# Optimization experiments

Measured on AMD Instinct MI355X. Metric: run time of the kernel, lower is better.

The kernel has to match this reference:

```python
import jax, jax.numpy as jnp
import numpy as np


def setup_inputs() -> dict:
    key = jax.random.key(0)
    ks = jax.random.split(key, 4)
    B, S, D, H, E = 4, 2048, 1024, 4096, 4
    sd = 1.0 / np.sqrt(D)
    sh = 1.0 / np.sqrt(H)
    return {
        "x": jax.random.normal(ks[0], (B, S, D), jnp.float32),
        "Wr": jax.random.normal(ks[1], (D, E), jnp.float32) * sd,
        "W1": jax.random.normal(ks[2], (E, D, H), jnp.float32) * sd,
        "b1": jnp.zeros((E, H), jnp.float32),
        "W2": jax.random.normal(ks[3], (E, H, D), jnp.float32) * sh,
        "b2": jnp.zeros((E, D), jnp.float32),
        "top_k": 2,
    }


def reference(x, Wr, W1, b1, W2, b2, top_k):
    # Router: softmax over experts, then top-k + renormalize (as in torch code)
    logits = jnp.einsum("bsd,de->bse", x, Wr)              # [B,S,E]
    probs = jax.nn.softmax(logits, axis=-1)
    wk, idx = jax.lax.top_k(probs, top_k)                  # [B,S,K]
    wk = wk / jnp.sum(wk, axis=-1, keepdims=True)
    # Scatter top-k weights back to dense per-expert weights [B,S,E]
    E = probs.shape[-1]
    onehot = jax.nn.one_hot(idx, E, dtype=x.dtype)         # [B,S,K,E]
    weights = jnp.einsum("bsk,bske->bse", wk, onehot)      # [B,S,E]
    # Expert MLPs (Linear-ReLU-Linear), computed dense over experts and
    # combined with the (mostly-zero) routing weights — same math as the
    # gather/scatter loop in the torch module.
    h = jax.nn.relu(jnp.einsum("bsd,edh->bseh", x, W1) + b1)   # [B,S,E,H]
    y = jnp.einsum("bseh,ehd->bsed", h, W2) + b2               # [B,S,E,D]
    out = jnp.einsum("bse,bsed->bsd", weights, y)              # [B,S,D]
    aux_loss = jnp.asarray(0.0, dtype=x.dtype)
    return out, aux_loss
```

## Files before the change

kernel.cpp:

```cpp
#include <hip/hip_runtime.h>
#include <cstdint>
#include <cstddef>

typedef _Float16 f16;
typedef __attribute__((ext_vector_type(8))) f16 f16x8;
typedef __attribute__((ext_vector_type(4))) f16 f16x4;
typedef __attribute__((ext_vector_type(4))) float f32x4;

#define M_TOK 8192
#define DDIM 1024
#define HDIM 4096
#define NEXP 4
#define TOTPAD 16896

__device__ __forceinline__ void async_copy16(const void* g, void* s) {
    __builtin_amdgcn_global_load_lds((__attribute__((address_space(1))) void*)g,
                                     (__attribute__((address_space(3))) void*)s,
                                     16, 0, 0);
}

__global__ __launch_bounds__(256) void router_kernel(
    const float* __restrict__ x, const float* __restrict__ Wr,
    float* __restrict__ wts, int* __restrict__ top2, float2* __restrict__ wpair) {
    __shared__ float wr_s[DDIM * NEXP];
    for (int i = threadIdx.x; i < DDIM * NEXP; i += 256) wr_s[i] = Wr[i];
    __syncthreads();
    const int wave = threadIdx.x >> 6, lane = threadIdx.x & 63;
    const int t = blockIdx.x * 4 + wave;
    float a0 = 0.f, a1 = 0.f, a2 = 0.f, a3 = 0.f;
    const float* xr = x + (size_t)t * DDIM;
    for (int i = 0; i < DDIM; i += 256) {
        const int d = i + lane * 4;
        const float4 v = *(const float4*)(xr + d);
        const float* w0 = &wr_s[d * 4];
        a0 += v.x * w0[0] + v.y * w0[4] + v.z * w0[8]  + v.w * w0[12];
        a1 += v.x * w0[1] + v.y * w0[5] + v.z * w0[9]  + v.w * w0[13];
        a2 += v.x * w0[2] + v.y * w0[6] + v.z * w0[10] + v.w * w0[14];
        a3 += v.x * w0[3] + v.y * w0[7] + v.z * w0[11] + v.w * w0[15];
    }
    for (int off = 32; off > 0; off >>= 1) {
        a0 += __shfl_xor(a0, off, 64);
        a1 += __shfl_xor(a1, off, 64);
        a2 += __shfl_xor(a2, off, 64);
        a3 += __shfl_xor(a3, off, 64);
    }
    if (lane == 0) {
        float lg[4] = {a0, a1, a2, a3};
        int i1 = 0;
        for (int e = 1; e < 4; ++e) if (lg[e] > lg[i1]) i1 = e;
        int i2 = -1;
        for (int e = 0; e < 4; ++e) {
            if (e == i1) continue;
            if (i2 < 0 || lg[e] > lg[i2]) i2 = e;
        }
        const float w1 = 1.0f / (1.0f + expf(lg[i2] - lg[i1]));
        float w[4] = {0.f, 0.f, 0.f, 0.f};
        w[i1] = w1; w[i2] = 1.0f - w1;
        float* o = wts + (size_t)t * 4;
        o[0] = w[0]; o[1] = w[1]; o[2] = w[2]; o[3] = w[3];
        top2[t] = i1 | (i2 << 8);
        wpair[t] = make_float2(w1, 1.0f - w1);
    }
}

__global__ __launch_bounds__(256) void count_kernel(
    const int* __restrict__ top2, int* __restrict__ meta) {
    __shared__ int lc[4];
    if (threadIdx.x < 4) lc[threadIdx.x] = 0;
    __syncthreads();
    const int t = blockIdx.x * 256 + threadIdx.x;
    const int p = top2[t];
    atomicAdd(&lc[p & 0xff], 1);
    atomicAdd(&lc[(p >> 8) & 0xff], 1);
    __syncthreads();
    if (threadIdx.x < 4) atomicAdd(&meta[threadIdx.x], lc[threadIdx.x]);
}

__global__ void offsets_kernel(int* __restrict__ meta) {
    if (threadIdx.x == 0) {
        int off = 0;
        for (int e = 0; e < 4; ++e) {
            const int c = meta[e];
            const int cp = (c + 127) & ~127;
            meta[4 + e] = cp;
            meta[8 + e] = off;
            off += cp;
        }
    }
}

__global__ __launch_bounds__(256) void fill_kernel(
    const int* __restrict__ top2, int* __restrict__ meta,
    int* __restrict__ toklist, int2* __restrict__ slotmap) {
    __shared__ int lc[4], base[4];
    if (threadIdx.x < 4) lc[threadIdx.x] = 0;
    __syncthreads();
    const int t = blockIdx.x * 256 + threadIdx.x;
    const int p = top2[t];
    const int e1 = p & 0xff, e2 = (p >> 8) & 0xff;
    const int r1 = atomicAdd(&lc[e1], 1);
    const int r2 = atomicAdd(&lc[e2], 1);
    __syncthreads();
    if (threadIdx.x < 4) base[threadIdx.x] = atomicAdd(&meta[12 + threadIdx.x], lc[threadIdx.x]);
    __syncthreads();
    const int p1 = meta[8 + e1] + base[e1] + r1;
    const int p2 = meta[8 + e2] + base[e2] + r2;
    toklist[p1] = t;
    toklist[p2] = t;
    slotmap[t] = make_int2(p1, p2);
}

__global__ __launch_bounds__(256) void convert_f16_kernel(
    const float* __restrict__ in, f16* __restrict__ out, int n4) {
    const int i = blockIdx.x * 256 + threadIdx.x;
    if (i < n4) {
        const float4 v = ((const float4*)in)[i];
        f16x4 o = {(f16)v.x, (f16)v.y, (f16)v.z, (f16)v.w};
        ((f16x4*)out)[i] = o;
    }
}

__global__ __launch_bounds__(256) void transpose_f16_kernel(
    const float* __restrict__ in0, f16* __restrict__ out0, int R, int C) {
    __shared__ float tile[32][33];
    const float* in = in0 + (size_t)blockIdx.z * R * C;
    f16* out = out0 + (size_t)blockIdx.z * R * C;
    const int c0 = blockIdx.x * 32, r0 = blockIdx.y * 32;
    const int tx = threadIdx.x & 31;
    const int ty = threadIdx.x >> 5;
#pragma unroll
    for (int i = 0; i < 32; i += 8)
        tile[ty + i][tx] = in[(size_t)(r0 + ty + i) * C + c0 + tx];
    __syncthreads();
#pragma unroll
    for (int i = 0; i < 32; i += 8)
        out[(size_t)(c0 + ty + i) * R + r0 + tx] = (f16)tile[tx][ty + i];
}

template <int MODE>
__global__ __launch_bounds__(256) void gemm_kernel(
    const f16* __restrict__ A, const f16* __restrict__ BT,
    int N, int K,
    const float* __restrict__ bias,
    f16* __restrict__ outH, float* __restrict__ outF,
    const float* __restrict__ wts,
    const int* __restrict__ toklist, const int* __restrict__ meta, int e0) {
    __shared__ __align__(16) f16 As[128 * 64];
    __shared__ __align__(16) f16 Bs[128 * 64];
    const int zz = blockIdx.z;
    const int e = e0 + zz;
    const int m0 = blockIdx.x * 128, n0 = blockIdx.y * 128;

    int cnt = M_TOK, off = 0;
    if (meta) {
        cnt = meta[e];
        const int cp = meta[4 + e];
        off = meta[8 + e];
        if (m0 >= cp) return;
    }

    const f16* BTe = BT + (size_t)zz * N * K;
    const float* be = bias + (size_t)zz * N;

    const int tid = threadIdx.x;
    const int wave = tid >> 6, lane = tid & 63;
    const int wm = wave >> 1, wn = wave & 1;
    const int quad = lane >> 4, l16 = lane & 15;

    f32x4 acc[4][4] = {};

    const int lrb = tid >> 3;
    const int gcoff = (((tid & 7) ^ (lrb & 7)) * 8);
    const f16* ga[4];
    const f16* gb[4];
#pragma unroll
    for (int r = 0; r < 4; ++r) {
        const int lr = r * 32 + lrb;
        const int gm = m0 + lr;
        int arow;
        if (MODE == 0) arow = toklist ? toklist[off + gm] : gm;
        else arow = off + gm;
        ga[r] = A + (size_t)arow * K + gcoff;
        gb[r] = BTe + (size_t)(n0 + lr) * K + gcoff;
    }

    const int swl = l16 & 7;
    for (int k0 = 0; k0 < K; k0 += 64) {
#pragma unroll
        for (int r = 0; r < 4; ++r)
            async_copy16(ga[r] + k0, &As[(r * 256 + tid) * 8]);
#pragma unroll
        for (int r = 0; r < 4; ++r)
            async_copy16(gb[r] + k0, &Bs[(r * 256 + tid) * 8]);
        __syncthreads();
#pragma unroll
        for (int kk = 0; kk < 64; kk += 32) {
            const int kc = kk >> 3;
            f16x8 af[4], bf[4];
#pragma unroll
            for (int i = 0; i < 4; ++i)
                af[i] = *(const f16x8*)&As[(size_t)(wm * 64 + i * 16 + l16) * 64 +
                                           (((kc + quad) ^ swl) << 3)];
#pragma unroll
            for (int j = 0; j < 4; ++j)
                bf[j] = *(const f16x8*)&Bs[(size_t)(wn * 64 + j * 16 + l16) * 64 +
                                           (((kc + quad) ^ swl) << 3)];
#pragma unroll
            for (int i = 0; i < 4; ++i)
#pragma unroll
                for (int j = 0; j < 4; ++j)
                    acc[i][j] = __builtin_amdgcn_mfma_f32_16x16x32_f16(af[i], bf[j], acc[i][j], 0, 0, 0);
        }
        __syncthreads();
    }

#pragma unroll
    for (int i = 0; i < 4; ++i) {
        const int mbase = m0 + wm * 64 + i * 16 + quad * 4;
#pragma unroll
        for (int j = 0; j < 4; ++j) {
            const int n = n0 + wn * 64 + j * 16 + l16;
            const float bv = be[n];
#pragma unroll
            for (int r = 0; r < 4; ++r) {
                const int m = mbase + r;
                float v = acc[i][j][r] + bv;
                if (MODE == 0) {
                    v = v > 0.0f ? v : 0.0f;
                    outH[(size_t)(off + m) * N + n] = (f16)v;
                } else {
                    if (outH) {
                        outH[(size_t)(off + m) * N + n] = (f16)v;
                    } else if (m < cnt) {
                        const float w = wts[m * 4 + e];
                        atomicAdd(&outF[(size_t)m * N + n], w * v);
                    }
                }
            }
        }
    }
}

__global__ __launch_bounds__(256) void combine_kernel(
    const f16* __restrict__ yseg, const int2* __restrict__ slotmap,
    const float2* __restrict__ wpair, float* __restrict__ out, int aux_idx) {
    const int t = blockIdx.x;
    const int2 p = slotmap[t];
    const float2 w = wpair[t];
    const int d = threadIdx.x * 4;
    const f16x4 a = *(const f16x4*)&yseg[(size_t)p.x * DDIM + d];
    const f16x4 b = *(const f16x4*)&yseg[(size_t)p.y * DDIM + d];
    float4 o;
    o.x = w.x * (float)a[0] + w.y * (float)b[0];
    o.y = w.x * (float)a[1] + w.y * (float)b[1];
    o.z = w.x * (float)a[2] + w.y * (float)b[2];
    o.w = w.x * (float)a[3] + w.y * (float)b[3];
    *(float4*)&out[(size_t)t * DDIM + d] = o;
    if (t == 0 && threadIdx.x == 0 && aux_idx >= 0) out[aux_idx] = 0.0f;
}

extern "C" void kernel_launch(void* const* d_in, const int* in_sizes, int n_in,
                              void* d_out, int out_size, void* d_ws, size_t ws_size,
                              hipStream_t stream) {
    (void)in_sizes; (void)n_in;
    const float* x  = (const float*)d_in[0];
    const float* Wr = (const float*)d_in[1];
    const float* W1 = (const float*)d_in[2];
    const float* b1 = (const float*)d_in[3];
    const float* W2 = (const float*)d_in[4];
    const float* b2 = (const float*)d_in[5];
    float* out = (float*)d_out;

    char* ws = (char*)d_ws;
    float*  wts   = (float*)ws;
    int*    meta  = (int*)(ws + (128 << 10));
    int*    top2  = (int*)(ws + (132 << 10));
    int*    tokl  = (int*)(ws + (164 << 10));
    float2* wpair = (float2*)(ws + (240 << 10));
    int2*   slotm = (int2*)(ws + (304 << 10));
    f16*    xb    = (f16*)(ws + (512 << 10));
    const size_t MBs = 1ull << 20;
    const size_t base = (512 << 10) + 16 * MBs;

    const size_t SPARSE_NEED = (512 << 10) + 80 * MBs + (size_t)TOTPAD * HDIM * sizeof(f16);
    const bool sparse = ws_size >= SPARSE_NEED;

    const int aux_idx = (out_size == M_TOK * DDIM + 1) ? (M_TOK * DDIM) : -1;

    f16 *w1t, *w2t, *h, *yseg;
    if (sparse) {
        w1t  = (f16*)(ws + base);
        w2t  = (f16*)(ws + base + 32 * MBs);
        h    = (f16*)(ws + base + 64 * MBs);
        yseg = (f16*)(ws + (512 << 10));
    } else {
        w1t = (f16*)(ws + base);
        w2t = (f16*)(ws + base + 8 * MBs);
        h   = (f16*)(ws + base + 16 * MBs);
        yseg = nullptr;
    }

    router_kernel<<<M_TOK / 4, 256, 0, stream>>>(x, Wr, wts, top2, wpair);
    convert_f16_kernel<<<(M_TOK * DDIM / 4) / 256, 256, 0, stream>>>(x, xb, M_TOK * DDIM / 4);

    if (sparse) {
        hipMemsetAsync(meta, 0, 16 * sizeof(int), stream);
        hipMemsetAsync(tokl, 0, (size_t)TOTPAD * sizeof(int), stream);
        count_kernel<<<M_TOK / 256, 256, 0, stream>>>(top2, meta);
        offsets_kernel<<<1, 64, 0, stream>>>(meta);
        fill_kernel<<<M_TOK / 256, 256, 0, stream>>>(top2, meta, tokl, slotm);
        transpose_f16_kernel<<<dim3(HDIM / 32, DDIM / 32, NEXP), 256, 0, stream>>>(W1, w1t, DDIM, HDIM);
        transpose_f16_kernel<<<dim3(DDIM / 32, HDIM / 32, NEXP), 256, 0, stream>>>(W2, w2t, HDIM, DDIM);
        gemm_kernel<0><<<dim3(M_TOK / 128, HDIM / 128, NEXP), 256, 0, stream>>>(
            xb, w1t, HDIM, DDIM, b1, h, nullptr, wts, tokl, meta, 0);
        gemm_kernel<1><<<dim3(M_TOK / 128, DDIM / 128, NEXP), 256, 0, stream>>>(
            h, w2t, DDIM, HDIM, b2, yseg, nullptr, wts, tokl, meta, 0);
        combine_kernel<<<M_TOK, 256, 0, stream>>>(yseg, slotm, wpair, out, aux_idx);
    } else {
        hipMemsetAsync(out, 0, (size_t)out_size * sizeof(float), stream);
        if (aux_idx < 0) {  }
        for (int e = 0; e < NEXP; ++e) {
            transpose_f16_kernel<<<dim3(HDIM / 32, DDIM / 32, 1), 256, 0, stream>>>(
                W1 + (size_t)e * DDIM * HDIM, w1t, DDIM, HDIM);
            gemm_kernel<0><<<dim3(M_TOK / 128, HDIM / 128, 1), 256, 0, stream>>>(
                xb, w1t, HDIM, DDIM, b1 + (size_t)e * HDIM, h, nullptr, wts, nullptr, nullptr, e);
            transpose_f16_kernel<<<dim3(DDIM / 32, HDIM / 32, 1), 256, 0, stream>>>(
                W2 + (size_t)e * HDIM * DDIM, w2t, HDIM, DDIM);
            gemm_kernel<1><<<dim3(M_TOK / 128, DDIM / 128, 1), 256, 0, stream>>>(
                h, w2t, DDIM, HDIM, b2 + (size_t)e * DDIM, nullptr, out, wts, nullptr, nullptr, e);
        }
    }
}
```

Measured before the change: 751.5 us.

## Double-buffer GEMM LDS tiles with register-staged prefetch of next K tile

```diff
diff --git a/kernel.cpp b/kernel.cpp
--- a/kernel.cpp
+++ b/kernel.cpp
@@ -6,18 +6,13 @@
 typedef __attribute__((ext_vector_type(8))) f16 f16x8;
 typedef __attribute__((ext_vector_type(4))) f16 f16x4;
 typedef __attribute__((ext_vector_type(4))) float f32x4;
+typedef __attribute__((ext_vector_type(4))) unsigned int u32x4;
 
 #define M_TOK 8192
 #define DDIM 1024
 #define HDIM 4096
 #define NEXP 4
 #define TOTPAD 16896
-
-__device__ __forceinline__ void async_copy16(const void* g, void* s) {
-    __builtin_amdgcn_global_load_lds((__attribute__((address_space(1))) void*)g,
-                                     (__attribute__((address_space(3))) void*)s,
-                                     16, 0, 0);
-}
 
 __global__ __launch_bounds__(256) void router_kernel(
     const float* __restrict__ x, const float* __restrict__ Wr,
@@ -138,15 +133,15 @@
 }
 
 template <int MODE>
-__global__ __launch_bounds__(256) void gemm_kernel(
+__global__ __launch_bounds__(256, 2) void gemm_kernel(
     const f16* __restrict__ A, const f16* __restrict__ BT,
     int N, int K,
     const float* __restrict__ bias,
     f16* __restrict__ outH, float* __restrict__ outF,
     const float* __restrict__ wts,
     const int* __restrict__ toklist, const int* __restrict__ meta, int e0) {
-    __shared__ __align__(16) f16 As[128 * 64];
-    __shared__ __align__(16) f16 Bs[128 * 64];
+    __shared__ __align__(16) f16 As[2][128 * 64];
+    __shared__ __align__(16) f16 Bs[2][128 * 64];
     const int zz = blockIdx.z;
     const int e = e0 + zz;
     const int m0 = blockIdx.x * 128, n0 = blockIdx.y * 128;
@@ -184,33 +179,49 @@
         gb[r] = BTe + (size_t)(n0 + lr) * K + gcoff;
     }
 
+    u32x4 ra[4], rb[4];
+#pragma unroll
+    for (int r = 0; r < 4; ++r) ra[r] = *(const u32x4*)(ga[r]);
+#pragma unroll
+    for (int r = 0; r < 4; ++r) rb[r] = *(const u32x4*)(gb[r]);
+#pragma unroll
+    for (int r = 0; r < 4; ++r) *(u32x4*)&As[0][(r * 256 + tid) * 8] = ra[r];
+#pragma unroll
+    for (int r = 0; r < 4; ++r) *(u32x4*)&Bs[0][(r * 256 + tid) * 8] = rb[r];
+    __syncthreads();
+
     const int swl = l16 & 7;
     for (int k0 = 0; k0 < K; k0 += 64) {
-#pragma unroll
-        for (int r = 0; r < 4; ++r)
-            async_copy16(ga[r] + k0, &As[(r * 256 + tid) * 8]);
-#pragma unroll
-        for (int r = 0; r < 4; ++r)
-            async_copy16(gb[r] + k0, &Bs[(r * 256 + tid) * 8]);
-        __syncthreads();
+        const int p = (k0 >> 6) & 1;
+        const int kn = (k0 + 64 < K) ? (k0 + 64) : 0;
+#pragma unroll
+        for (int r = 0; r < 4; ++r) ra[r] = *(const u32x4*)(ga[r] + kn);
+#pragma unroll
+        for (int r = 0; r < 4; ++r) rb[r] = *(const u32x4*)(gb[r] + kn);
+
 #pragma unroll
         for (int kk = 0; kk < 64; kk += 32) {
             const int kc = kk >> 3;
             f16x8 af[4], bf[4];
 #pragma unroll
             for (int i = 0; i < 4; ++i)
-                af[i] = *(const f16x8*)&As[(size_t)(wm * 64 + i * 16 + l16) * 64 +
-                                           (((kc + quad) ^ swl) << 3)];
+                af[i] = *(const f16x8*)&As[p][(size_t)(wm * 64 + i * 16 + l16) * 64 +
+                                             (((kc + quad) ^ swl) << 3)];
 #pragma unroll
             for (int j = 0; j < 4; ++j)
-                bf[j] = *(const f16x8*)&Bs[(size_t)(wn * 64 + j * 16 + l16) * 64 +
-                                           (((kc + quad) ^ swl) << 3)];
+                bf[j] = *(const f16x8*)&Bs[p][(size_t)(wn * 64 + j * 16 + l16) * 64 +
+                                             (((kc + quad) ^ swl) << 3)];
 #pragma unroll
             for (int i = 0; i < 4; ++i)
 #pragma unroll
                 for (int j = 0; j < 4; ++j)
                     acc[i][j] = __builtin_amdgcn_mfma_f32_16x16x32_f16(af[i], bf[j], acc[i][j], 0, 0, 0);
         }
+
+#pragma unroll
+        for (int r = 0; r < 4; ++r) *(u32x4*)&As[p ^ 1][(r * 256 + tid) * 8] = ra[r];
+#pragma unroll
+        for (int r = 0; r < 4; ++r) *(u32x4*)&Bs[p ^ 1][(r * 256 + tid) * 8] = rb[r];
         __syncthreads();
     }
 
@@ -318,7 +329,6 @@
         combine_kernel<<<M_TOK, 256, 0, stream>>>(yseg, slotm, wpair, out, aux_idx);
     } else {
         hipMemsetAsync(out, 0, (size_t)out_size * sizeof(float), stream);
-        if (aux_idx < 0) {  }
         for (int e = 0; e < NEXP; ++e) {
             transpose_f16_kernel<<<dim3(HDIM / 32, DDIM / 32, 1), 256, 0, stream>>>(
                 W1 + (size_t)e * DDIM * HDIM, w1t, DDIM, HDIM);
```

New measurement: 754.9 us. About the same (+0.5%).

## Pre-pack weights into MFMA fragment order and double-buffer A tiles

Applied to the files above, without the earlier changes.

```diff
diff --git a/kernel.cpp b/kernel.cpp
--- a/kernel.cpp
+++ b/kernel.cpp
@@ -120,33 +120,43 @@
     }
 }
 
-__global__ __launch_bounds__(256) void transpose_f16_kernel(
-    const float* __restrict__ in0, f16* __restrict__ out0, int R, int C) {
-    __shared__ float tile[32][33];
-    const float* in = in0 + (size_t)blockIdx.z * R * C;
-    f16* out = out0 + (size_t)blockIdx.z * R * C;
-    const int c0 = blockIdx.x * 32, r0 = blockIdx.y * 32;
-    const int tx = threadIdx.x & 31;
-    const int ty = threadIdx.x >> 5;
-#pragma unroll
-    for (int i = 0; i < 32; i += 8)
-        tile[ty + i][tx] = in[(size_t)(r0 + ty + i) * C + c0 + tx];
-    __syncthreads();
-#pragma unroll
-    for (int i = 0; i < 32; i += 8)
-        out[(size_t)(c0 + ty + i) * R + r0 + tx] = (f16)tile[tx][ty + i];
+__global__ __launch_bounds__(256) void pack_b_kernel(
+    const float* __restrict__ in0, f16* __restrict__ out0, int K, int N) {
+    __shared__ float tile[64][65];
+    const float* in = in0 + (size_t)blockIdx.z * K * N;
+    f16* out = out0 + (size_t)blockIdx.z * K * N;
+    const int n0 = blockIdx.x * 64, k0 = blockIdx.y * 64;
+    const int tx = threadIdx.x & 63, ty = threadIdx.x >> 6;
+#pragma unroll
+    for (int i = 0; i < 64; i += 4)
+        tile[ty + i][tx] = in[(size_t)(k0 + ty + i) * N + n0 + tx];
+    __syncthreads();
+#pragma unroll
+    for (int c = 0; c < 2; ++c) {
+        const int cc = c * 256 + threadIdx.x;
+        const int grp = cc >> 7;
+        const int within = cc & 127;
+        const int kk2 = within >> 6, quad = (within >> 4) & 3, l16 = within & 15;
+        const int nl = grp * 16 + l16;
+        const int kl = kk2 * 32 + quad * 8;
+        f16x8 v;
+#pragma unroll
+        for (int j = 0; j < 8; ++j) v[j] = (f16)tile[kl + j][nl];
+        const size_t o = ((size_t)(n0 / 16 + grp) * (K >> 6) + (k0 >> 6)) * 1024 +
+                         (size_t)within * 8;
+        *(f16x8*)&out[o] = v;
+    }
 }
 
 template <int MODE>
-__global__ __launch_bounds__(256) void gemm_kernel(
-    const f16* __restrict__ A, const f16* __restrict__ BT,
+__global__ __launch_bounds__(256, 3) void gemm_kernel(
+    const f16* __restrict__ A, const f16* __restrict__ Bswz,
     int N, int K,
     const float* __restrict__ bias,
     f16* __restrict__ outH, float* __restrict__ outF,
     const float* __restrict__ wts,
     const int* __restrict__ toklist, const int* __restrict__ meta, int e0) {
-    __shared__ __align__(16) f16 As[128 * 64];
-    __shared__ __align__(16) f16 Bs[128 * 64];
+    __shared__ __align__(16) f16 As[2][128 * 64];
     const int zz = blockIdx.z;
     const int e = e0 + zz;
     const int m0 = blockIdx.x * 128, n0 = blockIdx.y * 128;
@@ -159,59 +169,71 @@
         if (m0 >= cp) return;
     }
 
-    const f16* BTe = BT + (size_t)zz * N * K;
+    const f16* Be = Bswz + (size_t)zz * N * K;
     const float* be = bias + (size_t)zz * N;
 
     const int tid = threadIdx.x;
     const int wave = tid >> 6, lane = tid & 63;
     const int wm = wave >> 1, wn = wave & 1;
     const int quad = lane >> 4, l16 = lane & 15;
+    const int Kb = K >> 6;
 
     f32x4 acc[4][4] = {};
 
     const int lrb = tid >> 3;
     const int gcoff = (((tid & 7) ^ (lrb & 7)) * 8);
     const f16* ga[4];
-    const f16* gb[4];
 #pragma unroll
     for (int r = 0; r < 4; ++r) {
-        const int lr = r * 32 + lrb;
-        const int gm = m0 + lr;
+        const int gm = m0 + r * 32 + lrb;
         int arow;
         if (MODE == 0) arow = toklist ? toklist[off + gm] : gm;
         else arow = off + gm;
         ga[r] = A + (size_t)arow * K + gcoff;
-        gb[r] = BTe + (size_t)(n0 + lr) * K + gcoff;
-    }
+    }
+
+    const f16* bp[4];
+#pragma unroll
+    for (int j = 0; j < 4; ++j)
+        bp[j] = Be + ((size_t)(n0 / 16 + wn * 4 + j) * Kb) * 1024 + lane * 8;
+
+#pragma unroll
+    for (int r = 0; r < 4; ++r)
+        async_copy16(ga[r], &As[0][(r * 256 + tid) * 8]);
+    __syncthreads();
 
     const int swl = l16 & 7;
-    for (int k0 = 0; k0 < K; k0 += 64) {
-#pragma unroll
-        for (int r = 0; r < 4; ++r)
-            async_copy16(ga[r] + k0, &As[(r * 256 + tid) * 8]);
-#pragma unroll
-        for (int r = 0; r < 4; ++r)
-            async_copy16(gb[r] + k0, &Bs[(r * 256 + tid) * 8]);
+    int p = 0;
+    for (int k0b = 0; k0b < Kb; ++k0b) {
+        f16x8 bf[2][4];
+#pragma unroll
+        for (int kk2 = 0; kk2 < 2; ++kk2)
+#pragma unroll
+            for (int j = 0; j < 4; ++j)
+                bf[kk2][j] = *(const f16x8*)(bp[j] + (k0b << 10) + (kk2 << 9));
+
+        if (k0b + 1 < Kb) {
+            const int kn = (k0b + 1) << 6;
+#pragma unroll
+            for (int r = 0; r < 4; ++r)
+                async_copy16(ga[r] + kn, &As[p ^ 1][(r * 256 + tid) * 8]);
+        }
+
+#pragma unroll
+        for (int kk2 = 0; kk2 < 2; ++kk2) {
+            f16x8 af[4];
+#pragma unroll
+            for (int i = 0; i < 4; ++i)
+                af[i] = *(const f16x8*)&As[p][(size_t)(wm * 64 + i * 16 + l16) * 64 +
+                                             (((kk2 * 4 + quad) ^ swl) << 3)];
+#pragma unroll
+            for (int i = 0; i < 4; ++i)
+#pragma unroll
+                for (int j = 0; j < 4; ++j)
+                    acc[i][j] = __builtin_amdgcn_mfma_f32_16x16x32_f16(af[i], bf[kk2][j], acc[i][j], 0, 0, 0);
+        }
         __syncthreads();
-#pragma unroll
-        for (int kk = 0; kk < 64; kk += 32) {
-            const int kc = kk >> 3;
-            f16x8 af[4], bf[4];
-#pragma unroll
-            for (int i = 0; i < 4; ++i)
-                af[i] = *(const f16x8*)&As[(size_t)(wm * 64 + i * 16 + l16) * 64 +
-                                           (((kc + quad) ^ swl) << 3)];
-#pragma unroll
-            for (int j = 0; j < 4; ++j)
-                bf[j] = *(const f16x8*)&Bs[(size_t)(wn * 64 + j * 16 + l16) * 64 +
-                                           (((kc + quad) ^ swl) << 3)];
-#pragma unroll
-            for (int i = 0; i < 4; ++i)
-#pragma unroll
-                for (int j = 0; j < 4; ++j)
-                    acc[i][j] = __builtin_amdgcn_mfma_f32_16x16x32_f16(af[i], bf[j], acc[i][j], 0, 0, 0);
-        }
-        __syncthreads();
+        p ^= 1;
     }
 
 #pragma unroll
@@ -309,8 +331,8 @@
         count_kernel<<<M_TOK / 256, 256, 0, stream>>>(top2, meta);
         offsets_kernel<<<1, 64, 0, stream>>>(meta);
         fill_kernel<<<M_TOK / 256, 256, 0, stream>>>(top2, meta, tokl, slotm);
-        transpose_f16_kernel<<<dim3(HDIM / 32, DDIM / 32, NEXP), 256, 0, stream>>>(W1, w1t, DDIM, HDIM);
-        transpose_f16_kernel<<<dim3(DDIM / 32, HDIM / 32, NEXP), 256, 0, stream>>>(W2, w2t, HDIM, DDIM);
+        pack_b_kernel<<<dim3(HDIM / 64, DDIM / 64, NEXP), 256, 0, stream>>>(W1, w1t, DDIM, HDIM);
+        pack_b_kernel<<<dim3(DDIM / 64, HDIM / 64, NEXP), 256, 0, stream>>>(W2, w2t, HDIM, DDIM);
         gemm_kernel<0><<<dim3(M_TOK / 128, HDIM / 128, NEXP), 256, 0, stream>>>(
             xb, w1t, HDIM, DDIM, b1, h, nullptr, wts, tokl, meta, 0);
         gemm_kernel<1><<<dim3(M_TOK / 128, DDIM / 128, NEXP), 256, 0, stream>>>(
@@ -318,13 +340,12 @@
         combine_kernel<<<M_TOK, 256, 0, stream>>>(yseg, slotm, wpair, out, aux_idx);
     } else {
         hipMemsetAsync(out, 0, (size_t)out_size * sizeof(float), stream);
-        if (aux_idx < 0) {  }
         for (int e = 0; e < NEXP; ++e) {
-            transpose_f16_kernel<<<dim3(HDIM / 32, DDIM / 32, 1), 256, 0, stream>>>(
+            pack_b_kernel<<<dim3(HDIM / 64, DDIM / 64, 1), 256, 0, stream>>>(
                 W1 + (size_t)e * DDIM * HDIM, w1t, DDIM, HDIM);
             gemm_kernel<0><<<dim3(M_TOK / 128, HDIM / 128, 1), 256, 0, stream>>>(
                 xb, w1t, HDIM, DDIM, b1 + (size_t)e * HDIM, h, nullptr, wts, nullptr, nullptr, e);
-            transpose_f16_kernel<<<dim3(DDIM / 32, HDIM / 32, 1), 256, 0, stream>>>(
+            pack_b_kernel<<<dim3(DDIM / 64, HDIM / 64, 1), 256, 0, stream>>>(
                 W2 + (size_t)e * HDIM * DDIM, w2t, HDIM, DDIM);
             gemm_kernel<1><<<dim3(M_TOK / 128, DDIM / 128, 1), 256, 0, stream>>>(
                 h, w2t, DDIM, HDIM, b2 + (size_t)e * DDIM, nullptr, out, wts, nullptr, nullptr, e);
```

Measured after the change: 675.6 us. 1.11x faster.
